# Performance work log

Measured on AMD Instinct MI355X. Metric: run time of the kernel, lower is better.

Reference implementation:

```python
import jax, jax.numpy as jnp
import numpy as np

D_IN = 32
K = 16


def cbr(x, W, s, b):
    # 1x1 Conv2d + folded (eval-mode) BatchNorm + ReLU, channels-last.
    return jax.nn.relu(jnp.einsum('...i,io->...o', x, W) * s + b)


def gather_neighbour(pc, idx):
    # pc: [B, N, d]; idx: [B, N, K] -> [B, N, K, d]
    B, N, d = pc.shape
    g = jnp.take_along_axis(pc, idx.reshape(B, -1, 1), axis=1)
    return g.reshape(B, N, K, d)


def setup_inputs() -> dict:
    key = jax.random.key(0)
    ks = jax.random.split(key, 32)
    B, N = 2, 65536

    def w(k, ci, co):
        return jax.random.normal(k, (ci, co), jnp.float32) * (1.0 / np.sqrt(ci))

    inp = {
        'feature': jax.random.normal(ks[0], (B, D_IN, N, 1), jnp.float32),
        'xyz': jax.random.normal(ks[1], (B, N, 3), jnp.float32),
        'neigh_idx': jax.random.randint(ks[2], (B, N, K), 0, N, jnp.int64),
        # TNet
        'tW1': w(ks[3], 3, 16),  'ts1': jnp.ones(16),  'tb1': jnp.zeros(16),
        'tW2': w(ks[4], 16, 64), 'ts2': jnp.ones(64),  'tb2': jnp.zeros(64),
        'tW3': w(ks[5], 64, 16), 'ts3': jnp.ones(16),  'tb3': jnp.zeros(16),
        'tW4': w(ks[6], 16, 9),  'tb4': jnp.zeros(9),
        # RFA mlps
        'W1': w(ks[7], 3, 3),            's1': jnp.ones(3),     'b1': jnp.zeros(3),
        'W2': w(ks[8], D_IN, D_IN),      's2': jnp.ones(D_IN),  'b2': jnp.zeros(D_IN),
        'W3': w(ks[9], D_IN + 3, D_IN),  's3': jnp.ones(D_IN),  'b3': jnp.zeros(D_IN),
        'W4': w(ks[10], 2 * D_IN, D_IN), 's4': jnp.ones(D_IN),  'b4': jnp.zeros(D_IN),
    }
    return inp


def tnet(xyz, tW1, ts1, tb1, tW2, ts2, tb2, tW3, ts3, tb3, tW4, tb4):
    h = cbr(xyz, tW1, ts1, tb1)          # [B, N, 16]
    h = cbr(h, tW2, ts2, tb2)            # [B, N, 64]
    h = jnp.max(h, axis=1, keepdims=True)  # [B, 1, 64]
    h = cbr(h, tW3, ts3, tb3)            # [B, 1, 16]
    h = jnp.einsum('...i,io->...o', h, tW4) + tb4  # [B, 1, 9] (no bn/act)
    dia = jnp.eye(3, dtype=h.dtype).reshape(1, 1, 9)
    return (h + dia).reshape(-1, 3, 3)


def reference(feature, xyz, neigh_idx,
              tW1, ts1, tb1, tW2, ts2, tb2, tW3, ts3, tb3, tW4, tb4,
              W1, s1, b1, W2, s2, b2, W3, s3, b3, W4, s4, b4):
    # channels-last features [B, N, d_in]
    feat = feature.squeeze(-1).transpose(0, 2, 1)

    t = tnet(xyz, tW1, ts1, tb1, tW2, ts2, tb2, tW3, ts3, tb3, tW4, tb4)
    f_xyz = jnp.einsum('bni,bij->bnj', xyz, t)   # [B, N, 3]
    f_xyz = cbr(f_xyz, W1, s1, b1)               # [B, N, 3]
    f_xyz = gather_neighbour(f_xyz, neigh_idx)   # [B, N, K, 3]

    f_nei = cbr(feat, W2, s2, b2)                # [B, N, d]
    f_nei = gather_neighbour(f_nei, neigh_idx)   # [B, N, K, d]

    f_cat = jnp.concatenate([f_nei, f_xyz], axis=-1)  # [B, N, K, d+3]
    f_cat = cbr(f_cat, W3, s3, b3)               # [B, N, K, d]
    f_cat = jnp.max(f_cat, axis=2)               # max pooling over K -> [B, N, d]

    f = jnp.concatenate([feat, f_cat], axis=-1)  # [B, N, 2d]
    f = cbr(f, W4, s4, b4)                       # [B, N, d_in]
    return f.transpose(0, 2, 1)[..., None]       # [B, d_in, N, 1]
```

## Files before the change

kernel.cpp:

```cpp
#include <hip/hip_runtime.h>

#define NPTS   65536
#define TOTAL  (2 * NPTS)

typedef __attribute__((ext_vector_type(8)))  short short8;
typedef __attribute__((ext_vector_type(16))) float float16;
union F8 { uint4 u; short8 s; };

#define WS_STRIPE 0
#define WS_TG     262144
#define WS_T1A    262400
#define WS_T2     (262400 + TOTAL * 64)

__device__ __forceinline__ unsigned short f2bf(float x) {
    unsigned u = __float_as_uint(x);
    return (unsigned short)((u + 0x7FFFu + ((u >> 16) & 1u)) >> 16);
}
__device__ __forceinline__ unsigned pk2(float a, float b) {
    return (unsigned)f2bf(a) | ((unsigned)f2bf(b) << 16);
}
__device__ __forceinline__ float relu(float x) { return x > 0.f ? x : 0.f; }
__device__ __forceinline__ uint4 pk8(const float* e) {
    uint4 u;
    u.x = pk2(e[0], e[1]); u.y = pk2(e[2], e[3]);
    u.z = pk2(e[4], e[5]); u.w = pk2(e[6], e[7]);
    return u;
}
__device__ __forceinline__ float16 zero16() {
    float16 z;
#pragma unroll
    for (int i = 0; i < 16; i++) z[i] = 0.f;
    return z;
}

__global__ __launch_bounds__(256) void kA(
    const float* __restrict__ feature, const float* __restrict__ xyz,
    const float* __restrict__ tW1, const float* __restrict__ ts1, const float* __restrict__ tb1,
    const float* __restrict__ tW2, const float* __restrict__ ts2, const float* __restrict__ tb2,
    const float* __restrict__ W2,  const float* __restrict__ s2,  const float* __restrict__ b2,
    char* ws)
{
    __shared__ float red[4][64];
    float* stripe       = (float*)(ws + WS_STRIPE);
    unsigned short* t1a = (unsigned short*)(ws + WS_T1A);
    unsigned short* t2  = (unsigned short*)(ws + WS_T2);
    const int lane = threadIdx.x & 63, wv = threadIdx.x >> 6;
    const int col = lane & 31, h = lane >> 5;
    const float16 z = zero16();
    const int u = blockIdx.x;
    const int b = u >> 9;
    float e[8];
    float aw0[8], aw1[8], aw2[8], bb[8];
#pragma unroll
    for (int j = 0; j < 8; j++) {
        int k = 8 * h + j; float s = ts1[k];
        aw0[j] = tW1[k] * s; aw1[j] = tW1[16 + k] * s; aw2[j] = tW1[32 + k] * s;
        bb[j] = tb1[k];
    }
    F8 bf0, bf1;
#pragma unroll
    for (int j = 0; j < 8; j++) e[j] = tW2[(8 * h + j) * 64 + col] * ts2[col];
    bf0.u = pk8(e);
#pragma unroll
    for (int j = 0; j < 8; j++) e[j] = tW2[(8 * h + j) * 64 + 32 + col] * ts2[32 + col];
    bf1.u = pk8(e);
    F8 a0, a1;
    float sc2 = s2[col];
#pragma unroll
    for (int j = 0; j < 8; j++) e[j] = W2[(8 * h + j) * 32 + col] * sc2;
    a0.u = pk8(e);
#pragma unroll
    for (int j = 0; j < 8; j++) e[j] = W2[(16 + 8 * h + j) * 32 + col] * sc2;
    a1.u = pk8(e);
    float b2v[16];
#pragma unroll
    for (int r = 0; r < 16; r++) b2v[r] = b2[(r & 3) + 8 * (r >> 2) + 4 * h];

    int base = u * 128 + wv * 32;
    const float* xp = xyz + (size_t)(base + col) * 3;
    float x0 = xp[0], x1 = xp[1], x2 = xp[2];
    float hv[8];
#pragma unroll
    for (int j = 0; j < 8; j++)
        hv[j] = relu(x0 * aw0[j] + x1 * aw1[j] + x2 * aw2[j] + bb[j]);
    F8 af; af.u = pk8(hv);
    float16 c0 = __builtin_amdgcn_mfma_f32_32x32x16_bf16(af.s, bf0.s, z, 0, 0, 0);
    float16 c1 = __builtin_amdgcn_mfma_f32_32x32x16_bf16(af.s, bf1.s, z, 0, 0, 0);
    float v0 = c0[0], v1 = c1[0];
#pragma unroll
    for (int i = 1; i < 16; i++) { v0 = fmaxf(v0, c0[i]); v1 = fmaxf(v1, c1[i]); }
    v0 = fmaxf(v0, __shfl_xor(v0, 32));
    v1 = fmaxf(v1, __shfl_xor(v1, 32));
    if (h == 0) { red[wv][col] = v0; red[wv][32 + col] = v1; }
    __syncthreads();
    if (threadIdx.x < 64) {
        int c = threadIdx.x;
        float m = fmaxf(fmaxf(red[0][c], red[1][c]), fmaxf(red[2][c], red[3][c]));
        stripe[u * 64 + c] = relu(m + tb2[c]);
    }
    int pt = base + col;
    const float* fb = feature + (size_t)b * 32 * NPTS + (pt & (NPTS - 1));
    float v[8];
    F8 f0, f1;
#pragma unroll
    for (int j = 0; j < 8; j++) v[j] = fb[(size_t)(8 * h + j) * NPTS];
    f0.u = pk8(v);
#pragma unroll
    for (int j = 0; j < 8; j++) v[j] = fb[(size_t)(16 + 8 * h + j) * NPTS];
    f1.u = pk8(v);
    *(uint4*)(t2 + (size_t)pt * 32 + 8 * h) = f0.u;
    *(uint4*)(t2 + (size_t)pt * 32 + 16 + 8 * h) = f1.u;
    float16 acc = z;
    acc = __builtin_amdgcn_mfma_f32_32x32x16_bf16(a0.s, f0.s, acc, 0, 0, 0);
    acc = __builtin_amdgcn_mfma_f32_32x32x16_bf16(a1.s, f1.s, acc, 0, 0, 0);
#pragma unroll
    for (int q = 0; q < 4; q++) {
        int r = 4 * q;
        uint2 uu;
        uu.x = pk2(relu(acc[r] + b2v[r]), relu(acc[r + 1] + b2v[r + 1]));
        uu.y = pk2(relu(acc[r + 2] + b2v[r + 2]), relu(acc[r + 3] + b2v[r + 3]));
        *(uint2*)(t1a + (size_t)pt * 32 + 8 * q + 4 * h) = uu;
    }
}

__global__ __launch_bounds__(256) void kH(
    const float* __restrict__ tW3, const float* __restrict__ ts3, const float* __restrict__ tb3,
    const float* __restrict__ tW4, const float* __restrict__ tb4, char* ws)
{
    __shared__ float redh[4][64];
    const float* stripe = (const float*)(ws + WS_STRIPE);
    float* Tg           = (float*)(ws + WS_TG);
    const int batch = blockIdx.x;
    const int lane = threadIdx.x & 63, wv = threadIdx.x >> 6;
    {
        const float* sp = stripe + (size_t)(batch * 512 + wv * 128) * 64 + lane;
        float hm = 0.f;
#pragma unroll 8
        for (int s = 0; s < 128; s++) hm = fmaxf(hm, sp[s * 64]);
        redh[wv][lane] = hm;
    }
    __syncthreads();
    if (wv == 0) {
        float hm = fmaxf(fmaxf(redh[0][lane], redh[1][lane]),
                         fmaxf(redh[2][lane], redh[3][lane]));
        float v[16];
        const float4* trow = (const float4*)(tW3 + lane * 16);
#pragma unroll
        for (int q = 0; q < 4; q++) {
            float4 t4 = trow[q];
            v[4 * q + 0] = hm * t4.x; v[4 * q + 1] = hm * t4.y;
            v[4 * q + 2] = hm * t4.z; v[4 * q + 3] = hm * t4.w;
        }
#pragma unroll
        for (int off = 1; off < 64; off <<= 1) {
#pragma unroll
            for (int c = 0; c < 16; c++) v[c] += __shfl_xor(v[c], off);
        }
        float T[9];
#pragma unroll
        for (int j = 0; j < 9; j++) T[j] = tb4[j];
#pragma unroll
        for (int c = 0; c < 16; c++) {
            float h3 = relu(v[c] * ts3[c] + tb3[c]);
#pragma unroll
            for (int j = 0; j < 9; j++) T[j] += h3 * tW4[c * 9 + j];
        }
        T[0] += 1.f; T[4] += 1.f; T[8] += 1.f;
        if (lane < 9) Tg[batch * 16 + lane] = T[lane];
    }
}

__global__ __launch_bounds__(256) void kB(
    const float* __restrict__ xyz, const int* __restrict__ nidx,
    const float* __restrict__ W1,  const float* __restrict__ s1, const float* __restrict__ b1,
    const float* __restrict__ W3,  const float* __restrict__ s3, const float* __restrict__ b3,
    const float* __restrict__ W4,  const float* __restrict__ s4, const float* __restrict__ b4,
    char* ws, float* __restrict__ out)
{
    __shared__ unsigned short mld[64 * 36];
    const float* Tg           = (const float*)(ws + WS_TG);
    const unsigned short* t1a = (const unsigned short*)(ws + WS_T1A);
    const unsigned short* t2  = (const unsigned short*)(ws + WS_T2);
    const int lane = threadIdx.x & 63, wv = threadIdx.x >> 6;
    const int col = lane & 31, h = lane >> 5;
    const float16 z = zero16();

    int slot = blockIdx.x & 7, batch = slot >> 2;
    int grp = (blockIdx.x >> 3) * 4 + (slot & 3);
    int base = batch * NPTS + grp * 64;

    int idxs[8];
#pragma unroll
    for (int it = 0; it < 8; it++)
        idxs[it] = nidx[(base + 2 * (wv * 8 + it)) * 16 + col];

    float T[9];
#pragma unroll
    for (int j = 0; j < 9; j++) T[j] = Tg[batch * 16 + j];
    float W1f[9], b1v[3];
#pragma unroll
    for (int j = 0; j < 9; j++) W1f[j] = W1[j] * s1[j % 3];
#pragma unroll
    for (int j = 0; j < 3; j++) b1v[j] = b1[j];

    float e[8];
    F8 w0, w1, w2, zf;
    zf.u.x = zf.u.y = zf.u.z = zf.u.w = 0u;
    float sc3 = s3[col];
#pragma unroll
    for (int j = 0; j < 8; j++) e[j] = W3[(8 * h + j) * 32 + col] * sc3;
    w0.u = pk8(e);
#pragma unroll
    for (int j = 0; j < 8; j++) e[j] = W3[(16 + 8 * h + j) * 32 + col] * sc3;
    w1.u = pk8(e);
    w2 = zf;
    if (h == 0) {
        float e2[8] = {0.f, 0.f, 0.f, 0.f, 0.f, 0.f, 0.f, 0.f};
#pragma unroll
        for (int j = 0; j < 3; j++) e2[j] = W3[(32 + j) * 32 + col] * sc3;
        w2.u = pk8(e2);
    }
    float b3v = b3[col];

    F8 na0, na1;
    float nx0 = 0.f, nx1 = 0.f, nx2 = 0.f;
    {
        size_t row = ((size_t)batch << 16) + (unsigned)idxs[0];
        const unsigned short* ap = t1a + row * 32;
        na0.u = *(const uint4*)(ap + 8 * h);
        na1.u = *(const uint4*)(ap + 16 + 8 * h);
        if (h == 0) {
            const float* nxp = xyz + row * 3;
            nx0 = nxp[0]; nx1 = nxp[1]; nx2 = nxp[2];
        }
    }
    for (int it = 0; it < 8; it++) {
        F8 ca0 = na0, ca1 = na1;
        float cx0 = nx0, cx1 = nx1, cx2 = nx2;
        if (it < 7) {
            size_t row = ((size_t)batch << 16) + (unsigned)idxs[it + 1];
            const unsigned short* ap = t1a + row * 32;
            na0.u = *(const uint4*)(ap + 8 * h);
            na1.u = *(const uint4*)(ap + 16 + 8 * h);
            if (h == 0) {
                const float* nxp = xyz + row * 3;
                nx0 = nxp[0]; nx1 = nxp[1]; nx2 = nxp[2];
            }
        }
        F8 ca2 = zf;
        if (h == 0) {
            float q0 = cx0 * T[0] + cx1 * T[3] + cx2 * T[6];
            float q1 = cx0 * T[1] + cx1 * T[4] + cx2 * T[7];
            float q2 = cx0 * T[2] + cx1 * T[5] + cx2 * T[8];
            float r0 = relu(q0 * W1f[0] + q1 * W1f[3] + q2 * W1f[6] + b1v[0]);
            float r1 = relu(q0 * W1f[1] + q1 * W1f[4] + q2 * W1f[7] + b1v[1]);
            float r2 = relu(q0 * W1f[2] + q1 * W1f[5] + q2 * W1f[8] + b1v[2]);
            ca2.u.x = pk2(r0, r1); ca2.u.y = pk2(r2, 0.f);
        }
        float16 acc = z;
        acc = __builtin_amdgcn_mfma_f32_32x32x16_bf16(ca0.s, w0.s, acc, 0, 0, 0);
        acc = __builtin_amdgcn_mfma_f32_32x32x16_bf16(ca1.s, w1.s, acc, 0, 0, 0);
        acc = __builtin_amdgcn_mfma_f32_32x32x16_bf16(ca2.s, w2.s, acc, 0, 0, 0);
        float vA = acc[0], vB = acc[8];
#pragma unroll
        for (int r = 1; r < 8; r++) { vA = fmaxf(vA, acc[r]); vB = fmaxf(vB, acc[8 + r]); }
        vA = fmaxf(vA, __shfl_xor(vA, 32));
        vB = fmaxf(vB, __shfl_xor(vB, 32));
        vA = relu(vA + b3v);
        vB = relu(vB + b3v);
        float val = h ? vB : vA;
        int pl = 2 * (wv * 8 + it) + h;
        mld[pl * 36 + col] = f2bf(val);
    }
    __syncthreads();

    if (wv < 2) {
        F8 aw[4];
        float sc4 = s4[col];
#pragma unroll
        for (int t = 0; t < 4; t++) {
#pragma unroll
            for (int j = 0; j < 8; j++) e[j] = W4[(16 * t + 8 * h + j) * 32 + col] * sc4;
            aw[t].u = pk8(e);
        }
        float b4v[16];
#pragma unroll
        for (int r = 0; r < 16; r++) b4v[r] = b4[(r & 3) + 8 * (r >> 2) + 4 * h];
        int p_loc = wv * 32 + col;
        int p = base + p_loc;
        const unsigned short* bp = t2 + (size_t)p * 32 + 8 * h;
        F8 xf0, xf1;
        xf0.u = *(const uint4*)(bp);
        xf1.u = *(const uint4*)(bp + 16);
        const unsigned short* mp = mld + p_loc * 36;
        uint2 q0 = *(const uint2*)(mp + 8 * h);
        uint2 q1 = *(const uint2*)(mp + 8 * h + 4);
        uint2 q2 = *(const uint2*)(mp + 16 + 8 * h);
        uint2 q3 = *(const uint2*)(mp + 16 + 8 * h + 4);
        F8 xm0, xm1;
        xm0.u.x = q0.x; xm0.u.y = q0.y; xm0.u.z = q1.x; xm0.u.w = q1.y;
        xm1.u.x = q2.x; xm1.u.y = q2.y; xm1.u.z = q3.x; xm1.u.w = q3.y;
        float16 acc = z;
        acc = __builtin_amdgcn_mfma_f32_32x32x16_bf16(aw[0].s, xf0.s, acc, 0, 0, 0);
        acc = __builtin_amdgcn_mfma_f32_32x32x16_bf16(aw[1].s, xf1.s, acc, 0, 0, 0);
        acc = __builtin_amdgcn_mfma_f32_32x32x16_bf16(aw[2].s, xm0.s, acc, 0, 0, 0);
        acc = __builtin_amdgcn_mfma_f32_32x32x16_bf16(aw[3].s, xm1.s, acc, 0, 0, 0);
        float* ob = out + (size_t)(batch * 32) * NPTS + (p & (NPTS - 1));
#pragma unroll
        for (int r = 0; r < 16; r++) {
            int o = (r & 3) + 8 * (r >> 2) + 4 * h;
            ob[(size_t)o * NPTS] = relu(acc[r] + b4v[r]);
        }
    }
}

extern "C" void kernel_launch(void* const* d_in, const int* in_sizes, int n_in,
                              void* d_out, int out_size, void* d_ws, size_t ws_size,
                              hipStream_t stream)
{
    const float* feature = (const float*)d_in[0];
    const float* xyz     = (const float*)d_in[1];
    const int*   nidx    = (const int*)d_in[2];
    const float* tW1 = (const float*)d_in[3];
    const float* ts1 = (const float*)d_in[4];
    const float* tb1 = (const float*)d_in[5];
    const float* tW2 = (const float*)d_in[6];
    const float* ts2 = (const float*)d_in[7];
    const float* tb2 = (const float*)d_in[8];
    const float* tW3 = (const float*)d_in[9];
    const float* ts3 = (const float*)d_in[10];
    const float* tb3 = (const float*)d_in[11];
    const float* tW4 = (const float*)d_in[12];
    const float* tb4 = (const float*)d_in[13];
    const float* W1  = (const float*)d_in[14];
    const float* s1  = (const float*)d_in[15];
    const float* b1  = (const float*)d_in[16];
    const float* W2  = (const float*)d_in[17];
    const float* s2  = (const float*)d_in[18];
    const float* b2  = (const float*)d_in[19];
    const float* W3  = (const float*)d_in[20];
    const float* s3  = (const float*)d_in[21];
    const float* b3  = (const float*)d_in[22];
    const float* W4  = (const float*)d_in[23];
    const float* s4  = (const float*)d_in[24];
    const float* b4  = (const float*)d_in[25];
    (void)in_sizes; (void)n_in; (void)out_size; (void)ws_size;

    char* wsp = (char*)d_ws;
    float* outp = (float*)d_out;

    kA<<<1024, 256, 0, stream>>>(feature, xyz, tW1, ts1, tb1, tW2, ts2, tb2,
                                 W2, s2, b2, wsp);
    kH<<<2, 256, 0, stream>>>(tW3, ts3, tb3, tW4, tb4, wsp);
    kB<<<2048, 256, 0, stream>>>(xyz, nidx, W1, s1, b1, W3, s3, b3, W4, s4, b4,
                                 wsp, outp);
}
```

Before: 177.5 us.

## Fold TNet head kernel into main kernel via atomic max stripes

Result: faster. 165.6 us (-6.7%).

```diff
diff --git a/kernel.cpp b/kernel.cpp
--- a/kernel.cpp
+++ b/kernel.cpp
@@ -8,9 +8,8 @@
 union F8 { uint4 u; short8 s; };
 
 #define WS_STRIPE 0
-#define WS_TG     262144
-#define WS_T1A    262400
-#define WS_T2     (262400 + TOTAL * 64)
+#define WS_T1A    8192
+#define WS_T2     (8192 + TOTAL * 64)
 
 __device__ __forceinline__ unsigned short f2bf(float x) {
     unsigned u = __float_as_uint(x);
@@ -96,7 +95,8 @@
     if (threadIdx.x < 64) {
         int c = threadIdx.x;
         float m = fmaxf(fmaxf(red[0][c], red[1][c]), fmaxf(red[2][c], red[3][c]));
-        stripe[u * 64 + c] = relu(m + tb2[c]);
+        float val = relu(m + tb2[c]);
+        atomicMax((unsigned*)(stripe + (u & 15) * 128 + b * 64 + c), __float_as_uint(val));
     }
     int pt = base + col;
     const float* fb = feature + (size_t)b * 32 * NPTS + (pt & (NPTS - 1));
@@ -123,62 +123,17 @@
     }
 }
 
-__global__ __launch_bounds__(256) void kH(
-    const float* __restrict__ tW3, const float* __restrict__ ts3, const float* __restrict__ tb3,
-    const float* __restrict__ tW4, const float* __restrict__ tb4, char* ws)
-{
-    __shared__ float redh[4][64];
-    const float* stripe = (const float*)(ws + WS_STRIPE);
-    float* Tg           = (float*)(ws + WS_TG);
-    const int batch = blockIdx.x;
-    const int lane = threadIdx.x & 63, wv = threadIdx.x >> 6;
-    {
-        const float* sp = stripe + (size_t)(batch * 512 + wv * 128) * 64 + lane;
-        float hm = 0.f;
-#pragma unroll 8
-        for (int s = 0; s < 128; s++) hm = fmaxf(hm, sp[s * 64]);
-        redh[wv][lane] = hm;
-    }
-    __syncthreads();
-    if (wv == 0) {
-        float hm = fmaxf(fmaxf(redh[0][lane], redh[1][lane]),
-                         fmaxf(redh[2][lane], redh[3][lane]));
-        float v[16];
-        const float4* trow = (const float4*)(tW3 + lane * 16);
-#pragma unroll
-        for (int q = 0; q < 4; q++) {
-            float4 t4 = trow[q];
-            v[4 * q + 0] = hm * t4.x; v[4 * q + 1] = hm * t4.y;
-            v[4 * q + 2] = hm * t4.z; v[4 * q + 3] = hm * t4.w;
-        }
-#pragma unroll
-        for (int off = 1; off < 64; off <<= 1) {
-#pragma unroll
-            for (int c = 0; c < 16; c++) v[c] += __shfl_xor(v[c], off);
-        }
-        float T[9];
-#pragma unroll
-        for (int j = 0; j < 9; j++) T[j] = tb4[j];
-#pragma unroll
-        for (int c = 0; c < 16; c++) {
-            float h3 = relu(v[c] * ts3[c] + tb3[c]);
-#pragma unroll
-            for (int j = 0; j < 9; j++) T[j] += h3 * tW4[c * 9 + j];
-        }
-        T[0] += 1.f; T[4] += 1.f; T[8] += 1.f;
-        if (lane < 9) Tg[batch * 16 + lane] = T[lane];
-    }
-}
-
 __global__ __launch_bounds__(256) void kB(
     const float* __restrict__ xyz, const int* __restrict__ nidx,
+    const float* __restrict__ tW3, const float* __restrict__ ts3, const float* __restrict__ tb3,
+    const float* __restrict__ tW4, const float* __restrict__ tb4,
     const float* __restrict__ W1,  const float* __restrict__ s1, const float* __restrict__ b1,
     const float* __restrict__ W3,  const float* __restrict__ s3, const float* __restrict__ b3,
     const float* __restrict__ W4,  const float* __restrict__ s4, const float* __restrict__ b4,
     char* ws, float* __restrict__ out)
 {
     __shared__ unsigned short mld[64 * 36];
-    const float* Tg           = (const float*)(ws + WS_TG);
+    const float* stripe       = (const float*)(ws + WS_STRIPE);
     const unsigned short* t1a = (const unsigned short*)(ws + WS_T1A);
     const unsigned short* t2  = (const unsigned short*)(ws + WS_T2);
     const int lane = threadIdx.x & 63, wv = threadIdx.x >> 6;
@@ -195,8 +150,34 @@
         idxs[it] = nidx[(base + 2 * (wv * 8 + it)) * 16 + col];
 
     float T[9];
-#pragma unroll
-    for (int j = 0; j < 9; j++) T[j] = Tg[batch * 16 + j];
+    {
+        float hm = 0.f;
+#pragma unroll
+        for (int s = 0; s < 16; s++)
+            hm = fmaxf(hm, stripe[s * 128 + batch * 64 + lane]);
+        float v[16];
+        const float4* trow = (const float4*)(tW3 + lane * 16);
+#pragma unroll
+        for (int q = 0; q < 4; q++) {
+            float4 t4 = trow[q];
+            v[4 * q + 0] = hm * t4.x; v[4 * q + 1] = hm * t4.y;
+            v[4 * q + 2] = hm * t4.z; v[4 * q + 3] = hm * t4.w;
+        }
+#pragma unroll
+        for (int off = 1; off < 64; off <<= 1) {
+#pragma unroll
+            for (int c = 0; c < 16; c++) v[c] += __shfl_xor(v[c], off);
+        }
+#pragma unroll
+        for (int j = 0; j < 9; j++) T[j] = tb4[j];
+#pragma unroll
+        for (int c = 0; c < 16; c++) {
+            float h3 = relu(v[c] * ts3[c] + tb3[c]);
+#pragma unroll
+            for (int j = 0; j < 9; j++) T[j] += h3 * tW4[c * 9 + j];
+        }
+        T[0] += 1.f; T[4] += 1.f; T[8] += 1.f;
+    }
     float W1f[9], b1v[3];
 #pragma unroll
     for (int j = 0; j < 9; j++) W1f[j] = W1[j] * s1[j % 3];
@@ -349,9 +330,9 @@
     char* wsp = (char*)d_ws;
     float* outp = (float*)d_out;
 
+    hipMemsetAsync(wsp + WS_STRIPE, 0, 16 * 128 * sizeof(float), stream);
     kA<<<1024, 256, 0, stream>>>(feature, xyz, tW1, ts1, tb1, tW2, ts2, tb2,
                                  W2, s2, b2, wsp);
-    kH<<<2, 256, 0, stream>>>(tW3, ts3, tb3, tW4, tb4, wsp);
-    kB<<<2048, 256, 0, stream>>>(xyz, nidx, W1, s1, b1, W3, s3, b3, W4, s4, b4,
-                                 wsp, outp);
-}
+    kB<<<2048, 256, 0, stream>>>(xyz, nidx, tW3, ts3, tb3, tW4, tb4,
+                                 W1, s1, b1, W3, s3, b3, W4, s4, b4, wsp, outp);
+}
```
